# Kernel tuning notes

Measured on AMD Instinct MI355X. Metric: run time of the kernel, lower is better.

Reference implementation:

```python
import jax, jax.numpy as jnp
import numpy as np

B, C, CI, H, W = 16, 256, 128, 64, 64


def setup_inputs() -> dict:
    key = jax.random.key(0)
    k1, k2, k3, k4, k5, k6 = jax.random.split(key, 6)
    x_gallery = jax.random.normal(k1, (B, C, H, W), dtype=jnp.float32)
    x_query = jax.random.normal(k2, (B, C, H, W), dtype=jnp.float32)
    # 1x1 conv weights (kernel_size=1 -> equivalent to per-pixel linear map)
    s = 1.0 / np.sqrt(C)
    theta_w = jax.random.uniform(k3, (CI, C), jnp.float32, -s, s)
    theta_b = jax.random.uniform(k4, (CI,), jnp.float32, -s, s)
    phi_w = jax.random.uniform(k5, (CI, C), jnp.float32, -s, s)
    phi_b = jax.random.uniform(k6, (CI,), jnp.float32, -s, s)
    return {"x_gallery": x_gallery, "x_query": x_query,
            "theta_w": theta_w, "theta_b": theta_b,
            "phi_w": phi_w, "phi_b": phi_b}


def reference(x_gallery, x_query, theta_w, theta_b, phi_w, phi_b):
    b, c, h, w = x_gallery.shape
    # 1x1 convs == channel-mixing einsum
    theta_x = jnp.einsum('bchw,oc->bohw', x_gallery, theta_w) + theta_b[None, :, None, None]
    phi_x = jnp.einsum('bchw,oc->bohw', x_query, phi_w) + phi_b[None, :, None, None]
    t = theta_x.reshape(b, theta_x.shape[1], -1)   # [B, CI, HW]
    p = phi_x.reshape(b, phi_x.shape[1], -1)       # [B, CI, H'W']
    n = p.shape[-1]
    # f[b, i, j] = <theta[:, i], phi[:, j]> / N   (norm == 'size')
    f = jnp.einsum('bci,bcj->bij', t, p) / n       # [B, HW, H'W']
    f = jnp.max(f, axis=2)                         # row-wise max (non-softmax attention)
    f = f.reshape(b, 1, h, w)
    return jax.nn.sigmoid(f)                       # message == 'attention_map'
```

## Files before the change

### kernel.cpp

```cpp
#include <hip/hip_runtime.h>
#include <hip/hip_bf16.h>

#define B_   16
#define CIN  256
#define CO   128
#define HW   4096

typedef __attribute__((ext_vector_type(8))) short short8;
typedef __attribute__((ext_vector_type(4))) float f32x4;
typedef __attribute__((ext_vector_type(4))) unsigned u32x4;

__device__ __forceinline__ short f32_to_bf16_rne(float f) {
    union { float f; unsigned u; } v; v.f = f;
    unsigned u = v.u;
    u += 0x7fffu + ((u >> 16) & 1u);
    return (short)(u >> 16);
}

__device__ __forceinline__ unsigned pack_bf16(float lo, float hi) {
    return (unsigned)(unsigned short)f32_to_bf16_rne(lo) |
           ((unsigned)(unsigned short)f32_to_bf16_rne(hi) << 16);
}

__global__ __launch_bounds__(256) void wconv_kernel(
    const float* __restrict__ tw, const float* __restrict__ pw,
    short* __restrict__ wbf)
{
    const int idx = blockIdx.x * 256 + threadIdx.x;
    const float v = (idx < CO * CIN) ? tw[idx] : pw[idx - CO * CIN];
    wbf[idx] = f32_to_bf16_rne(v);
}

__global__ __launch_bounds__(256, 3) void proj_kernel(
    const float* __restrict__ xg, const float* __restrict__ xq,
    const float* __restrict__ tb, const float* __restrict__ pb,
    const short* __restrict__ wbf,
    short* __restrict__ tT, short* __restrict__ pT)
{
    const int n     = blockIdx.x;
    const int xcd   = n & 7;
    const int q     = n >> 3;
    const int itile = q & 63;
    const int rr    = q >> 6;
    const int which = rr & 1;
    const int b     = xcd + 8 * (rr >> 1);

    const float* x    = which ? xq : xg;
    const float* bias = which ? pb : tb;
    const short* wb   = wbf + which * CO * CIN;
    short*       out  = which ? pT : tT;

    const int i0   = itile * 64;
    const int tid  = threadIdx.x;
    const int lane = tid & 63;
    const int wv   = tid >> 6;
    const int nrow = lane & 15;
    const int quad = lane >> 4;

    const int iq   = (tid & 15) * 4;
    const int g    = tid >> 4;
    const int swz  = tid & 15;

    __shared__ __align__(16) short xT[2][64][128];

    f32x4 acc[4][2] = {};

    float bias_v[2];
    bias_v[0] = bias[wv * 32 + 0  + nrow];
    bias_v[1] = bias[wv * 32 + 16 + nrow];

    const float* xb = x + (long)b * CIN * HW + i0;

    float4 lv[8];
    auto stage_load = [&](int c) {
        const float* src = xb + (long)(c * 128 + g * 8) * HW + iq;
        #pragma unroll
        for (int r = 0; r < 8; r++)
            lv[r] = *(const float4*)(src + (long)r * HW);
    };
    auto stage_write = [&](int buf) {
        const int ck = (g ^ swz) * 8;
        #pragma unroll
        for (int k = 0; k < 4; k++) {
            u32x4 d;
            const float* f = (const float*)lv;
            #pragma unroll
            for (int p = 0; p < 4; p++)
                d[p] = pack_bf16(f[(2 * p) * 4 + k], f[(2 * p + 1) * 4 + k]);
            *(u32x4*)&xT[buf][iq + k][ck] = d;
        }
    };

    short8 wf[2][4][2];
    auto wload = [&](int c, int buf) {
        #pragma unroll
        for (int ks = 0; ks < 4; ks++)
            #pragma unroll
            for (int nt = 0; nt < 2; nt++)
                wf[buf][ks][nt] = *(const short8*)(
                    wb + (wv * 32 + nt * 16 + nrow) * CIN + c * 128 + ks * 32 + quad * 8);
    };

    auto compute = [&](int buf) {
        #pragma unroll
        for (int ks = 0; ks < 4; ks++)
            #pragma unroll
            for (int mt = 0; mt < 4; mt++) {
                const int row = mt * 16 + nrow;
                const int ck  = ((ks * 4 + quad) ^ ((row >> 2) & 15)) * 8;
                const short8 a = *(const short8*)&xT[buf][row][ck];
                acc[mt][0] = __builtin_amdgcn_mfma_f32_16x16x32_bf16(a, wf[buf][ks][0], acc[mt][0], 0, 0, 0);
                acc[mt][1] = __builtin_amdgcn_mfma_f32_16x16x32_bf16(a, wf[buf][ks][1], acc[mt][1], 0, 0, 0);
            }
    };

    wload(0, 0);
    stage_load(0);
    stage_write(0);
    __syncthreads();
    stage_load(1);
    wload(1, 1);
    compute(0);
    stage_write(1);
    __syncthreads();
    compute(1);

    #pragma unroll
    for (int mt = 0; mt < 4; mt++)
        #pragma unroll
        for (int nt = 0; nt < 2; nt++) {
            const int co = wv * 32 + nt * 16 + nrow;
            #pragma unroll
            for (int r = 0; r < 4; r++) {
                const int il = mt * 16 + quad * 4 + r;
                out[((long)b * HW + i0 + il) * CO + co] =
                    f32_to_bf16_rne(acc[mt][nt][r] + bias_v[nt]);
            }
        }
}

__global__ __launch_bounds__(256, 2) void maxgemm_kernel(
    const short* __restrict__ tT, const short* __restrict__ pT,
    float* __restrict__ pmax)
{
    const int n     = blockIdx.x;
    const int b     = (n & 7) + 8 * ((n >> 3) & 1);
    const int mm    = n >> 4;
    const int itile = mm & 7;
    const int jq    = mm >> 3;
    const int i0    = itile * 512;
    const int j0    = jq * 1024;
    const int tid   = threadIdx.x;
    const int lane  = tid & 63;
    const int wv    = tid >> 6;
    const int nrow  = lane & 15;
    const int quad  = lane >> 4;

    __shared__ short bT[2][64][128];

    short8 afrag[8][4];
    {
        const short* ta = tT + ((long)b * HW + i0 + wv * 128) * CO;
        #pragma unroll
        for (int mt = 0; mt < 8; mt++)
            #pragma unroll
            for (int ks = 0; ks < 4; ks++)
                afrag[mt][ks] = *(const short8*)(ta + (mt * 16 + nrow) * CO + ks * 32 + quad * 8);
    }

    const short* pb2 = pT + (long)b * HW * CO + (long)j0 * CO;
    const int sc8 = tid & 15;
    const int sj0 = tid >> 4;

    short8 sreg[4];
    auto stage_load = [&](int jt) {
        const short* src = pb2 + (long)jt * 64 * CO;
        #pragma unroll
        for (int r = 0; r < 4; r++)
            sreg[r] = *(const short8*)(src + (sj0 + r * 16) * CO + sc8 * 8);
    };
    auto stage_write = [&](int buf) {
        #pragma unroll
        for (int r = 0; r < 4; r++) {
            const int j  = sj0 + r * 16;
            const int c8 = sc8 ^ (j & 7);
            *(short8*)&bT[buf][j][c8 * 8] = sreg[r];
        }
    };

    f32x4 vmax[8];
    #pragma unroll
    for (int mt = 0; mt < 8; mt++)
        vmax[mt] = (f32x4){-1e30f, -1e30f, -1e30f, -1e30f};

    const f32x4 kz = {0.f, 0.f, 0.f, 0.f};

    auto compute = [&](int buf) {
        #pragma unroll
        for (int np = 0; np < 2; np++) {
            short8 bf0[4], bf1[4];
            const int ja = np * 32 + nrow;
            const int jb = ja + 16;
            #pragma unroll
            for (int ks = 0; ks < 4; ks++) {
                bf0[ks] = *(const short8*)&bT[buf][ja][(((ks * 4 + quad) ^ (ja & 7)) * 8)];
                bf1[ks] = *(const short8*)&bT[buf][jb][(((ks * 4 + quad) ^ (jb & 7)) * 8)];
            }
            #pragma unroll
            for (int mt = 0; mt < 8; mt++) {
                f32x4 a0 = __builtin_amdgcn_mfma_f32_16x16x32_bf16(afrag[mt][0], bf0[0], kz, 0, 0, 0);
                f32x4 a1 = __builtin_amdgcn_mfma_f32_16x16x32_bf16(afrag[mt][0], bf1[0], kz, 0, 0, 0);
                #pragma unroll
                for (int ks = 1; ks < 4; ks++) {
                    a0 = __builtin_amdgcn_mfma_f32_16x16x32_bf16(afrag[mt][ks], bf0[ks], a0, 0, 0, 0);
                    a1 = __builtin_amdgcn_mfma_f32_16x16x32_bf16(afrag[mt][ks], bf1[ks], a1, 0, 0, 0);
                }
                #pragma unroll
                for (int r = 0; r < 4; r++)
                    vmax[mt][r] = fmaxf(fmaxf(a0[r], a1[r]), vmax[mt][r]);
            }
        }
    };

    stage_load(0);
    stage_write(0);
    for (int jt = 0; jt < 16; jt++) {
        __syncthreads();
        if (jt < 15) stage_load(jt + 1);
        compute(jt & 1);
        if (jt < 15) stage_write((jt + 1) & 1);
    }

    #pragma unroll
    for (int mt = 0; mt < 8; mt++)
        #pragma unroll
        for (int r = 0; r < 4; r++) {
            float v = vmax[mt][r];
            #pragma unroll
            for (int m = 8; m >= 1; m >>= 1)
                v = fmaxf(v, __shfl_xor(v, m, 64));
            vmax[mt][r] = v;
        }

    if (nrow == 0) {
        float* pm = pmax + (size_t)jq * (B_ * HW) + (size_t)b * HW + i0 + wv * 128;
        #pragma unroll
        for (int mt = 0; mt < 8; mt++)
            #pragma unroll
            for (int r = 0; r < 4; r++)
                pm[mt * 16 + quad * 4 + r] = vmax[mt][r];
    }
}

__global__ __launch_bounds__(256) void combine_kernel(
    const float* __restrict__ pmax, float* __restrict__ out)
{
    const int idx = blockIdx.x * 256 + threadIdx.x;
    float v = pmax[idx];
    #pragma unroll
    for (int p = 1; p < 4; p++)
        v = fmaxf(v, pmax[idx + p * (B_ * HW)]);
    v *= (1.0f / (float)HW);
    out[idx] = 1.0f / (1.0f + __expf(-v));
}

extern "C" void kernel_launch(void* const* d_in, const int* in_sizes, int n_in,
                              void* d_out, int out_size, void* d_ws, size_t ws_size,
                              hipStream_t stream) {
    const float* xg = (const float*)d_in[0];
    const float* xq = (const float*)d_in[1];
    const float* tw = (const float*)d_in[2];
    const float* tb = (const float*)d_in[3];
    const float* pw = (const float*)d_in[4];
    const float* pb = (const float*)d_in[5];
    float* out = (float*)d_out;

    short* tT  = (short*)d_ws;
    short* pT  = tT + (size_t)B_ * HW * CO;
    short* wbf = pT + (size_t)B_ * HW * CO;
    float* pmax = (float*)(wbf + 2 * CO * CIN);

    wconv_kernel<<<(2 * CO * CIN) / 256, 256, 0, stream>>>(tw, pw, wbf);
    proj_kernel<<<B_ * (HW / 64) * 2, 256, 0, stream>>>(xg, xq, tb, pb, wbf, tT, pT);
    maxgemm_kernel<<<B_ * (HW / 512) * 4, 256, 0, stream>>>(tT, pT, pmax);
    combine_kernel<<<(B_ * HW) / 256, 256, 0, stream>>>(pmax, out);
}
```

Baseline: 226.8 us.

## Stage projection inputs and weights via global_load_lds with 4-stage K pipeline

Rewrites the projection kernel to copy fp32 activation tiles and bf16 weight tiles directly from global memory into LDS with global_load_lds. The bf16 conversion moves into the compute loop, and K is split into four 64-channel chunks with double buffering. Each wave now owns 16 pixels across all 128 output channels instead of 32 channels across 64 pixels. This removes the register round trip and the pack-before-store step when staging, but it uses more LDS (fp32 tile) and targets 2 blocks per CU instead of 3. Reading the activations from LDS uses scalar strided loads, which may cause bank conflicts.

```diff
diff --git a/kernel.cpp b/kernel.cpp
--- a/kernel.cpp
+++ b/kernel.cpp
@@ -22,6 +22,12 @@
            ((unsigned)(unsigned short)f32_to_bf16_rne(hi) << 16);
 }
 
+__device__ __forceinline__ void gload16(const void* g, void* l) {
+    __builtin_amdgcn_global_load_lds(
+        (const __attribute__((address_space(1))) void*)g,
+        (__attribute__((address_space(3))) void*)l, 16, 0, 0);
+}
+
 __global__ __launch_bounds__(256) void wconv_kernel(
     const float* __restrict__ tw, const float* __restrict__ pw,
     short* __restrict__ wbf)
@@ -31,7 +37,7 @@
     wbf[idx] = f32_to_bf16_rne(v);
 }
 
-__global__ __launch_bounds__(256, 3) void proj_kernel(
+__global__ __launch_bounds__(256, 2) void proj_kernel(
     const float* __restrict__ xg, const float* __restrict__ xq,
     const float* __restrict__ tb, const float* __restrict__ pb,
     const short* __restrict__ wbf,
@@ -57,86 +63,80 @@
     const int nrow = lane & 15;
     const int quad = lane >> 4;
 
-    const int iq   = (tid & 15) * 4;
-    const int g    = tid >> 4;
-    const int swz  = tid & 15;
-
-    __shared__ __align__(16) short xT[2][64][128];
-
-    f32x4 acc[4][2] = {};
-
-    float bias_v[2];
-    bias_v[0] = bias[wv * 32 + 0  + nrow];
-    bias_v[1] = bias[wv * 32 + 16 + nrow];
+    __shared__ __align__(16) float ftile[2][16][260];
+    __shared__ __align__(16) short wtile[2][128][64];
 
     const float* xb = x + (long)b * CIN * HW + i0;
-
-    float4 lv[8];
-    auto stage_load = [&](int c) {
-        const float* src = xb + (long)(c * 128 + g * 8) * HW + iq;
-        #pragma unroll
-        for (int r = 0; r < 8; r++)
-            lv[r] = *(const float4*)(src + (long)r * HW);
-    };
-    auto stage_write = [&](int buf) {
-        const int ck = (g ^ swz) * 8;
-        #pragma unroll
-        for (int k = 0; k < 4; k++) {
-            u32x4 d;
-            const float* f = (const float*)lv;
+    auto stage_x = [&](int c, int buf) {
+        #pragma unroll
+        for (int s = 0; s < 4; s++) {
+            const int g = wv * 4 + s;
+            const float* gsrc = xb + (long)(c * 64 + g * 4 + (lane >> 4)) * HW + (lane & 15) * 4;
+            gload16(gsrc, &ftile[buf][g][0]);
+        }
+    };
+    auto stage_w = [&](int c, int buf) {
+        #pragma unroll
+        for (int s = 0; s < 4; s++) {
+            const int g  = wv * 4 + s;
+            const int co = g * 8 + (lane >> 3);
+            const int ck = (lane & 7) ^ (co & 7);
+            const short* gsrc = wb + (long)co * CIN + c * 64 + ck * 8;
+            gload16(gsrc, &wtile[buf][g * 8][0]);
+        }
+    };
+
+    f32x4 acc[8] = {};
+
+    float bias_v[8];
+    #pragma unroll
+    for (int nt = 0; nt < 8; nt++)
+        bias_v[nt] = bias[nt * 16 + nrow];
+
+    auto compute = [&](int buf) {
+        #pragma unroll
+        for (int ks = 0; ks < 2; ks++) {
+            float af[8];
+            #pragma unroll
+            for (int r = 0; r < 8; r++) {
+                const int ci = ks * 32 + quad * 8 + r;
+                af[r] = ftile[buf][ci >> 2][(ci & 3) * 64 + wv * 16 + nrow];
+            }
+            u32x4 ap;
             #pragma unroll
             for (int p = 0; p < 4; p++)
-                d[p] = pack_bf16(f[(2 * p) * 4 + k], f[(2 * p + 1) * 4 + k]);
-            *(u32x4*)&xT[buf][iq + k][ck] = d;
-        }
-    };
-
-    short8 wf[2][4][2];
-    auto wload = [&](int c, int buf) {
-        #pragma unroll
-        for (int ks = 0; ks < 4; ks++)
-            #pragma unroll
-            for (int nt = 0; nt < 2; nt++)
-                wf[buf][ks][nt] = *(const short8*)(
-                    wb + (wv * 32 + nt * 16 + nrow) * CIN + c * 128 + ks * 32 + quad * 8);
-    };
-
-    auto compute = [&](int buf) {
-        #pragma unroll
-        for (int ks = 0; ks < 4; ks++)
-            #pragma unroll
-            for (int mt = 0; mt < 4; mt++) {
-                const int row = mt * 16 + nrow;
-                const int ck  = ((ks * 4 + quad) ^ ((row >> 2) & 15)) * 8;
-                const short8 a = *(const short8*)&xT[buf][row][ck];
-                acc[mt][0] = __builtin_amdgcn_mfma_f32_16x16x32_bf16(a, wf[buf][ks][0], acc[mt][0], 0, 0, 0);
-                acc[mt][1] = __builtin_amdgcn_mfma_f32_16x16x32_bf16(a, wf[buf][ks][1], acc[mt][1], 0, 0, 0);
-            }
-    };
-
-    wload(0, 0);
-    stage_load(0);
-    stage_write(0);
+                ap[p] = pack_bf16(af[2 * p], af[2 * p + 1]);
+            const short8 a = *(const short8*)&ap;
+            #pragma unroll
+            for (int nt = 0; nt < 8; nt++) {
+                const int co = nt * 16 + nrow;
+                const int sw = (ks * 4 + quad) ^ (co & 7);
+                const short8 bw = *(const short8*)&wtile[buf][co][sw * 8];
+                acc[nt] = __builtin_amdgcn_mfma_f32_16x16x32_bf16(a, bw, acc[nt], 0, 0, 0);
+            }
+        }
+    };
+
+    stage_x(0, 0);
+    stage_w(0, 0);
     __syncthreads();
-    stage_load(1);
-    wload(1, 1);
-    compute(0);
-    stage_write(1);
-    __syncthreads();
-    compute(1);
-
-    #pragma unroll
-    for (int mt = 0; mt < 4; mt++)
-        #pragma unroll
-        for (int nt = 0; nt < 2; nt++) {
-            const int co = wv * 32 + nt * 16 + nrow;
-            #pragma unroll
-            for (int r = 0; r < 4; r++) {
-                const int il = mt * 16 + quad * 4 + r;
-                out[((long)b * HW + i0 + il) * CO + co] =
-                    f32_to_bf16_rne(acc[mt][nt][r] + bias_v[nt]);
-            }
-        }
+    #pragma unroll
+    for (int c = 0; c < 4; c++) {
+        if (c < 3) { stage_x(c + 1, (c + 1) & 1); stage_w(c + 1, (c + 1) & 1); }
+        compute(c & 1);
+        __syncthreads();
+    }
+
+    #pragma unroll
+    for (int nt = 0; nt < 8; nt++) {
+        const int co = nt * 16 + nrow;
+        #pragma unroll
+        for (int r = 0; r < 4; r++) {
+            const int il = wv * 16 + quad * 4 + r;
+            out[((long)b * HW + i0 + il) * CO + co] =
+                f32_to_bf16_rne(acc[nt][r] + bias_v[nt]);
+        }
+    }
 }
 
 __global__ __launch_bounds__(256, 2) void maxgemm_kernel(
```

Result: faster. 220.7 us (-2.7%).
